# Performance work log

Measured on AMD Instinct MI355X. Metric: run time of the kernel, lower is better.

The kernel has to match this reference:

```python
import jax, jax.numpy as jnp
import numpy as np

SCALE_FACTOR = 4.0
DROPOUT_P = 0.5
DROPOUT_KEY = jax.random.key(42)  # fixed key: torch dropout is stochastic; we fix RNG for reproducibility


def setup_inputs() -> dict:
    key = jax.random.key(0)
    k1, k2 = jax.random.split(key)
    x1 = jax.random.normal(k1, (4096, 1024), dtype=jnp.float32)
    x2 = jax.random.normal(k2, (4096, 1024), dtype=jnp.float32)
    return {"x1": x1, "x2": x2}


def reference(x1, x2):
    # scores: [M, N] = x1 @ x2^T, scaled
    scores = jnp.matmul(x1, x2.T) * SCALE_FACTOR
    # F.softmax with no dim on 2-D input -> softmax over dim 1 (keys)
    attn = jax.nn.softmax(scores, axis=-1)
    # dropout p=0.5, train mode (inverted dropout: scale kept units by 1/(1-p))
    keep = jax.random.bernoulli(DROPOUT_KEY, 1.0 - DROPOUT_P, attn.shape)
    attn = jnp.where(keep, attn / (1.0 - DROPOUT_P), 0.0).astype(attn.dtype)
    # output: [M, D] = attn @ x2 (x2 reused as values)
    return jnp.matmul(attn, x2)
```

## Files before the change

### kernel.cpp

```cpp
#include <hip/hip_runtime.h>

typedef unsigned short u16;
typedef unsigned int   u32;
typedef __attribute__((ext_vector_type(4))) float f32x4;
typedef __attribute__((ext_vector_type(8))) short bf16x8;
typedef __attribute__((ext_vector_type(8))) unsigned short u16x8;
typedef __attribute__((ext_vector_type(4))) unsigned short u16x4;

#define MROWS 4096
#define DDIM  1024

__device__ __forceinline__ u16 f2bf(float f) {
  u32 u = __float_as_uint(f);
  return (u16)((u + 0x7FFFu + ((u >> 16) & 1u)) >> 16);
}
__device__ __forceinline__ float bf2f(u16 h) { return __uint_as_float(((u32)h) << 16); }

__device__ __forceinline__ u32 rotl32(u32 x, int r) { return (x << r) | (x >> (32 - r)); }
__device__ __forceinline__ u32 threefry_bits(u32 n) {
  const u32 K0 = 0u, K1 = 42u, K2 = 0x1BD11BDAu ^ 0u ^ 42u;
  u32 x0 = K0;
  u32 x1 = n + K1;
#define TF4(a,b,c,d) \
  x0 += x1; x1 = rotl32(x1, a); x1 ^= x0; \
  x0 += x1; x1 = rotl32(x1, b); x1 ^= x0; \
  x0 += x1; x1 = rotl32(x1, c); x1 ^= x0; \
  x0 += x1; x1 = rotl32(x1, d); x1 ^= x0;
  TF4(13,15,26,6);  x0 += K1; x1 += K2 + 1u;
  TF4(17,29,16,24); x0 += K2; x1 += K0 + 2u;
  TF4(13,15,26,6);  x0 += K0; x1 += K1 + 3u;
  TF4(17,29,16,24); x0 += K1; x1 += K2 + 4u;
  TF4(13,15,26,6);  x0 += K2; x1 += K0 + 5u;
#undef TF4
  return x0 ^ x1;
}

__global__ __launch_bounds__(256)
void expand3(const float4* __restrict__ x, u16* __restrict__ out, float scale, int patA,
             u32* __restrict__ mask, u32 wordBase) {
  int t = blockIdx.x * 256 + threadIdx.x;
  float4 v0 = x[(size_t)t * 2], v1 = x[(size_t)t * 2 + 1];
  float vv[8] = {v0.x*scale, v0.y*scale, v0.z*scale, v0.w*scale,
                 v1.x*scale, v1.y*scale, v1.z*scale, v1.w*scale};
  u16 o[24];
#pragma unroll
  for (int j = 0; j < 8; ++j) {
    u16 h = f2bf(vv[j]);
    u16 l = f2bf(vv[j] - bf2f(h));
    if (patA) { o[3*j]=h; o[3*j+1]=h; o[3*j+2]=l; }
    else      { o[3*j]=h; o[3*j+1]=l; o[3*j+2]=h; }
  }
  u16x8* dst = (u16x8*)(out + (size_t)t * 24);
#pragma unroll
  for (int q = 0; q < 3; ++q) {
    u16x8 wv;
#pragma unroll
    for (int j = 0; j < 8; ++j) wv[j] = o[q*8+j];
    dst[q] = wv;
  }
  u32 w = wordBase + ((u32)t >> 1);
  u32 sh = ((u32)t & 1u) << 4;
  u32 n0 = w * 32u + sh;
  u32 half = 0;
#pragma unroll 4
  for (int b = 0; b < 16; ++b) half |= (threefry_bits(n0 + (u32)b) >> 31) << (sh + b);
  u32 word = half | (u32)__shfl_xor((int)half, 1, 64);
  if ((t & 1) == 0) mask[w] = word;
}

__global__ __launch_bounds__(256)
void transpose_bf16(const float* __restrict__ x2, u16* __restrict__ VT) {
  __shared__ float tile[64][65];
  int tid = threadIdx.x;
  int dt = blockIdx.x;
  int kt = blockIdx.y;
#pragma unroll
  for (int it = 0; it < 16; ++it) {
    int lin = it * 256 + tid;
    int r = lin >> 6, c = lin & 63;
    tile[r][c] = x2[(size_t)(kt*64 + r) * DDIM + dt*64 + c];
  }
  __syncthreads();
#pragma unroll
  for (int it = 0; it < 16; ++it) {
    int lin = it * 256 + tid;
    int dr = lin >> 6, kc = lin & 63;
    VT[(size_t)(dt*64 + dr) * MROWS + kt*64 + kc] = f2bf(tile[kc][dr]);
  }
}

__device__ __forceinline__ void gload16(const u16* g, u16* l) {
  __builtin_amdgcn_global_load_lds(
      (const __attribute__((address_space(1))) void*)g,
      (__attribute__((address_space(3))) void*)l, 16, 0, 0);
}

#define BARRIER() do { asm volatile("" ::: "memory"); __builtin_amdgcn_s_barrier(); \
                       asm volatile("" ::: "memory"); } while (0)
#define VMCNT(N)  asm volatile("s_waitcnt vmcnt(" #N ")" ::: "memory")
#define PRIO1()   __builtin_amdgcn_s_setprio(1)
#define PRIO0()   __builtin_amdgcn_s_setprio(0)

__device__ __forceinline__ void mma_quad(f32x4 (&acc)[8][4], const bf16x8 (&aF)[4][2],
                                         const bf16x8 (&bF)[2][2], int MH, int NH) {
#pragma unroll
  for (int kx = 0; kx < 2; ++kx)
#pragma unroll
    for (int m = 0; m < 4; ++m)
#pragma unroll
      for (int n = 0; n < 2; ++n)
        acc[MH*4+m][NH*2+n] = __builtin_amdgcn_mfma_f32_16x16x32_bf16(
            aF[m][kx], bF[n][kx], acc[MH*4+m][NH*2+n], 0, 0, 0);
}

template <bool OUT16>
__global__ __launch_bounds__(512, 2)
void gemm256(const u16* __restrict__ A, const u16* __restrict__ Bt, void* __restrict__ Cv,
             int M, int N, int K, int ntpc) {
  __shared__ u16 smem[65536];
  const int tid = threadIdx.x;
  const int lane = tid & 63;
  const int w = tid >> 6;
  const int wr = w >> 2;
  const int wc = w & 3;
  const int fr = lane & 15;
  const int hi = lane >> 4;

  const long bm = (long)blockIdx.y * 256;
  const long bn = (long)blockIdx.x * 256;
  const size_t kcol0 = (size_t)blockIdx.z * ntpc * 64;

  const int srow = tid >> 3;
  const int scol = (((tid & 7) ^ (srow & 7)) << 3);
  const u16* Abase = A  + (size_t)(bm + srow) * K + kcol0 + scol;
  const u16* Bbase = Bt + (size_t)(bn + srow) * K + kcol0 + scol;

  const int csw0 = ((hi)     ^ (fr & 7)) << 3;
  const int csw1 = ((4 + hi) ^ (fr & 7)) << 3;
  const int arow = (wr*16 + fr) * 64;
  const int brow = (wc*16 + fr) * 64;

#define RD_A(dst, D, H) do { \
    const u16* _b0 = smem + ((D)*2+(H))*8192 + arow + csw0; \
    const u16* _b1 = smem + ((D)*2+(H))*8192 + arow + csw1; \
    dst[0][0] = *(const bf16x8*)(_b0);        dst[0][1] = *(const bf16x8*)(_b1); \
    dst[1][0] = *(const bf16x8*)(_b0 + 2048); dst[1][1] = *(const bf16x8*)(_b1 + 2048); \
    dst[2][0] = *(const bf16x8*)(_b0 + 4096); dst[2][1] = *(const bf16x8*)(_b1 + 4096); \
    dst[3][0] = *(const bf16x8*)(_b0 + 6144); dst[3][1] = *(const bf16x8*)(_b1 + 6144); } while (0)
#define RD_B(dst, D, H) do { \
    const u16* _b0 = smem + 32768 + ((D)*2+(H))*8192 + brow + csw0; \
    const u16* _b1 = smem + 32768 + ((D)*2+(H))*8192 + brow + csw1; \
    dst[0][0] = *(const bf16x8*)(_b0);        dst[0][1] = *(const bf16x8*)(_b1); \
    dst[1][0] = *(const bf16x8*)(_b0 + 4096); dst[1][1] = *(const bf16x8*)(_b1 + 4096); } while (0)

  f32x4 acc[8][4];
#pragma unroll
  for (int m = 0; m < 8; ++m)
#pragma unroll
    for (int n = 0; n < 4; ++n) acc[m][n] = (f32x4){0.f, 0.f, 0.f, 0.f};
  bf16x8 a0[4][2], a1[4][2], b0[2][2], b1[2][2];

#define STAGE_A(TAU,H,D) do { \
    const u16* _s = Abase + (size_t)(H)*128*K + (size_t)(TAU)*64; \
    u16* _d = smem + ((D)*2+(H))*8192 + tid*8; \
    gload16(_s, _d); gload16(_s + (size_t)64*K, _d + 4096); } while (0)
#define STAGE_B(TAU,H,D) do { \
    const u16* _s = Bbase + (size_t)(H)*128*K + (size_t)(TAU)*64; \
    u16* _d = smem + 32768 + ((D)*2+(H))*8192 + tid*8; \
    gload16(_s, _d); gload16(_s + (size_t)64*K, _d + 4096); } while (0)

  STAGE_A(0,0,0); STAGE_B(0,0,0);
  VMCNT(0); BARRIER();
  RD_A(a0, 0, 0); RD_B(b0, 0, 0);
  STAGE_B(0,1,0);
  STAGE_A(0,1,0);
  STAGE_A(1,0,1); STAGE_B(1,0,1);
  STAGE_B(1,1,1);
  STAGE_A(1,1,1);
  VMCNT(10); BARRIER();

  const int nt = ntpc;
  for (int T = 0; T < nt; T += 2) {
    const int t2 = (T + 2 < nt) ? T + 2 : nt - 1;
    const int t3 = (T + 3 < nt) ? T + 3 : nt - 1;

    RD_B(b1, 0, 1);
    PRIO1(); mma_quad(acc, a0, b0, 0, 0); PRIO0();
    VMCNT(8);  BARRIER();
    RD_A(a1, 0, 1);
    STAGE_A(t2, 0, 0); STAGE_B(t2, 0, 0);
    PRIO1(); mma_quad(acc, a0, b1, 0, 1); PRIO0();
    BARRIER();
    STAGE_B(t2, 1, 0);
    PRIO1(); mma_quad(acc, a1, b0, 1, 0); PRIO0();
    VMCNT(10); BARRIER();
    RD_A(a0, 1, 0); RD_B(b0, 1, 0);
    STAGE_A(t2, 1, 0);
    PRIO1(); mma_quad(acc, a1, b1, 1, 1); PRIO0();
    VMCNT(10); BARRIER();
    RD_B(b1, 1, 1);
    PRIO1(); mma_quad(acc, a0, b0, 0, 0); PRIO0();
    VMCNT(8);  BARRIER();
    RD_A(a1, 1, 1);
    STAGE_A(t3, 0, 1); STAGE_B(t3, 0, 1);
    PRIO1(); mma_quad(acc, a0, b1, 0, 1); PRIO0();
    BARRIER();
    STAGE_B(t3, 1, 1);
    PRIO1(); mma_quad(acc, a1, b0, 1, 0); PRIO0();
    VMCNT(10); BARRIER();
    RD_A(a0, 0, 0); RD_B(b0, 0, 0);
    STAGE_A(t3, 1, 1);
    PRIO1(); mma_quad(acc, a1, b1, 1, 1); PRIO0();
    VMCNT(10); BARRIER();
  }
#undef STAGE_A
#undef STAGE_B
#undef RD_A
#undef RD_B

#pragma unroll
  for (int m = 0; m < 8; ++m)
#pragma unroll
    for (int n = 0; n < 4; ++n) {
      size_t row0 = (size_t)(bm + m*32 + wr*16 + hi*4);
      size_t col  = (size_t)(bn + n*64 + wc*16 + fr);
#pragma unroll
      for (int r = 0; r < 4; ++r) {
        if (OUT16) {
          u16* Cz = (u16*)Cv + (size_t)blockIdx.z * (size_t)M * N;
          Cz[(row0 + r) * N + col] = f2bf(acc[m][n][r]);
        } else {
          float* Cz = (float*)Cv + (size_t)blockIdx.z * (size_t)M * N;
          Cz[(row0 + r) * N + col] = acc[m][n][r];
        }
      }
    }
}

__global__ __launch_bounds__(256)
void softmax_dropout(const float* __restrict__ S, const u32* __restrict__ mask,
                     u16* __restrict__ P) {
  const int tid  = threadIdx.x;
  const int lane = tid & 63;
  const int w    = tid >> 6;
  const int row  = blockIdx.x * 4 + w;
  const float4* Sr = (const float4*)(S + (size_t)row * MROWS);
  float4 v[16];
#pragma unroll
  for (int i = 0; i < 16; ++i) v[i] = Sr[i * 64 + lane];
  float m = -3.0e38f;
#pragma unroll
  for (int i = 0; i < 16; ++i)
    m = fmaxf(m, fmaxf(fmaxf(v[i].x, v[i].y), fmaxf(v[i].z, v[i].w)));
#pragma unroll
  for (int off = 32; off > 0; off >>= 1) m = fmaxf(m, __shfl_xor(m, off, 64));
  float s = 0.0f;
#pragma unroll
  for (int i = 0; i < 16; ++i) {
    v[i].x = __expf(v[i].x - m); v[i].y = __expf(v[i].y - m);
    v[i].z = __expf(v[i].z - m); v[i].w = __expf(v[i].w - m);
    s += v[i].x + v[i].y + v[i].z + v[i].w;
  }
#pragma unroll
  for (int off = 32; off > 0; off >>= 1) s += __shfl_xor(s, off, 64);
  const float inv = 2.0f / s;
  u16* Pr = P + (size_t)row * MROWS;
  const u32* Mw = mask + (size_t)row * 128;
#pragma unroll
  for (int i = 0; i < 16; ++i) {
    int j0 = (i * 64 + lane) * 4;
    u32 word = Mw[j0 >> 5];
    int sh = j0 & 31;
    float e[4] = {v[i].x, v[i].y, v[i].z, v[i].w};
    u16x4 o;
#pragma unroll
    for (int c = 0; c < 4; ++c) {
      float val = ((word >> (sh + c)) & 1u) ? 0.0f : e[c] * inv;
      o[c] = f2bf(val);
    }
    *(u16x4*)(Pr + j0) = o;
  }
}

__global__ __launch_bounds__(256)
void reduce4(const u16* __restrict__ p, float4* __restrict__ out) {
  size_t i = (size_t)blockIdx.x * 256 + threadIdx.x;
  const size_t NP = (size_t)MROWS * DDIM;
  u16x4 a = *(const u16x4*)(p + i*4);
  u16x4 b = *(const u16x4*)(p + NP + i*4);
  u16x4 c = *(const u16x4*)(p + 2*NP + i*4);
  u16x4 d = *(const u16x4*)(p + 3*NP + i*4);
  float4 r;
  r.x = bf2f(a[0]) + bf2f(b[0]) + bf2f(c[0]) + bf2f(d[0]);
  r.y = bf2f(a[1]) + bf2f(b[1]) + bf2f(c[1]) + bf2f(d[1]);
  r.z = bf2f(a[2]) + bf2f(b[2]) + bf2f(c[2]) + bf2f(d[2]);
  r.w = bf2f(a[3]) + bf2f(b[3]) + bf2f(c[3]) + bf2f(d[3]);
  out[i] = r;
}

extern "C" void kernel_launch(void* const* d_in, const int* in_sizes, int n_in,
                              void* d_out, int out_size, void* d_ws, size_t ws_size,
                              hipStream_t stream) {
  const float* x1 = (const float*)d_in[0];
  const float* x2 = (const float*)d_in[1];
  float* out = (float*)d_out;
  char* ws = (char*)d_ws;

  const size_t OFF_XB   = 25165824;
  const size_t OFF_VT   = 50331648;
  const size_t OFF_S    = 58720256;
  const size_t OFF_MASK = 125829120;
  const size_t NEED     = 127926272;
  if (ws_size < NEED) {
    hipMemsetAsync(d_out, 0x7F, (size_t)out_size * sizeof(float), stream);
    return;
  }
  u16*   XA = (u16*)(ws);
  u16*   XB = (u16*)(ws + OFF_XB);
  u16*   VT = (u16*)(ws + OFF_VT);
  float* S  = (float*)(ws + OFF_S);
  u16*   PT = (u16*)(ws + OFF_S);
  u32*   MK = (u32*)(ws + OFF_MASK);
  u16*   P  = (u16*)(ws);

  expand3<<<2048, 256, 0, stream>>>((const float4*)x1, XA, 4.0f, 1, MK, 0u);
  expand3<<<2048, 256, 0, stream>>>((const float4*)x2, XB, 1.0f, 0, MK, 262144u);
  transpose_bf16<<<dim3(16, 64), 256, 0, stream>>>(x2, VT);
  gemm256<false><<<dim3(16, 16, 1), 512, 0, stream>>>(XA, XB, S, 4096, 4096, 3072, 48);
  softmax_dropout<<<1024, 256, 0, stream>>>(S, MK, P);
  gemm256<true><<<dim3(4, 16, 4), 512, 0, stream>>>(P, VT, PT, 4096, 1024, 4096, 16);
  reduce4<<<4096, 256, 0, stream>>>(PT, (float4*)out);
}
```

Measured before the change: 192.0 us.

## Generate dropout mask inline in softmax, fuse x2 cast with transpose, remap PV grid

```diff
diff --git a/kernel.cpp b/kernel.cpp
--- a/kernel.cpp
+++ b/kernel.cpp
@@ -36,19 +36,17 @@
 }
 
 __global__ __launch_bounds__(256)
-void expand3(const float4* __restrict__ x, u16* __restrict__ out, float scale, int patA,
-             u32* __restrict__ mask, u32 wordBase) {
+void expandA(const float4* __restrict__ x, u16* __restrict__ out) {
   int t = blockIdx.x * 256 + threadIdx.x;
   float4 v0 = x[(size_t)t * 2], v1 = x[(size_t)t * 2 + 1];
-  float vv[8] = {v0.x*scale, v0.y*scale, v0.z*scale, v0.w*scale,
-                 v1.x*scale, v1.y*scale, v1.z*scale, v1.w*scale};
+  float vv[8] = {v0.x*4.f, v0.y*4.f, v0.z*4.f, v0.w*4.f,
+                 v1.x*4.f, v1.y*4.f, v1.z*4.f, v1.w*4.f};
   u16 o[24];
 #pragma unroll
   for (int j = 0; j < 8; ++j) {
     u16 h = f2bf(vv[j]);
     u16 l = f2bf(vv[j] - bf2f(h));
-    if (patA) { o[3*j]=h; o[3*j+1]=h; o[3*j+2]=l; }
-    else      { o[3*j]=h; o[3*j+1]=l; o[3*j+2]=h; }
+    o[3*j] = h; o[3*j+1] = h; o[3*j+2] = l;
   }
   u16x8* dst = (u16x8*)(out + (size_t)t * 24);
 #pragma unroll
@@ -58,18 +56,11 @@
     for (int j = 0; j < 8; ++j) wv[j] = o[q*8+j];
     dst[q] = wv;
   }
-  u32 w = wordBase + ((u32)t >> 1);
-  u32 sh = ((u32)t & 1u) << 4;
-  u32 n0 = w * 32u + sh;
-  u32 half = 0;
-#pragma unroll 4
-  for (int b = 0; b < 16; ++b) half |= (threefry_bits(n0 + (u32)b) >> 31) << (sh + b);
-  u32 word = half | (u32)__shfl_xor((int)half, 1, 64);
-  if ((t & 1) == 0) mask[w] = word;
 }
 
 __global__ __launch_bounds__(256)
-void transpose_bf16(const float* __restrict__ x2, u16* __restrict__ VT) {
+void castB_transpose(const float* __restrict__ x2, u16* __restrict__ XB,
+                     u16* __restrict__ VT) {
   __shared__ float tile[64][65];
   int tid = threadIdx.x;
   int dt = blockIdx.x;
@@ -81,6 +72,27 @@
     tile[r][c] = x2[(size_t)(kt*64 + r) * DDIM + dt*64 + c];
   }
   __syncthreads();
+#pragma unroll
+  for (int itr = 0; itr < 2; ++itr) {
+    int r  = (tid >> 3) + itr * 32;
+    int c0 = (tid & 7) * 8;
+    u16 o[24];
+#pragma unroll
+    for (int j = 0; j < 8; ++j) {
+      float v = tile[r][c0 + j];
+      u16 h = f2bf(v);
+      u16 l = f2bf(v - bf2f(h));
+      o[3*j] = h; o[3*j+1] = l; o[3*j+2] = h;
+    }
+    u16x8* dst = (u16x8*)(XB + (size_t)(kt*64 + r) * 3072 + (size_t)(dt*64 + c0) * 3);
+#pragma unroll
+    for (int q = 0; q < 3; ++q) {
+      u16x8 wv;
+#pragma unroll
+      for (int j = 0; j < 8; ++j) wv[j] = o[q*8+j];
+      dst[q] = wv;
+    }
+  }
 #pragma unroll
   for (int it = 0; it < 16; ++it) {
     int lin = it * 256 + tid;
@@ -113,7 +125,7 @@
             aF[m][kx], bF[n][kx], acc[MH*4+m][NH*2+n], 0, 0, 0);
 }
 
-template <bool OUT16>
+template <bool OUT16, bool REMAP>
 __global__ __launch_bounds__(512, 2)
 void gemm256(const u16* __restrict__ A, const u16* __restrict__ Bt, void* __restrict__ Cv,
              int M, int N, int K, int ntpc) {
@@ -126,8 +138,18 @@
   const int fr = lane & 15;
   const int hi = lane >> 4;
 
-  const long bm = (long)blockIdx.y * 256;
-  const long bn = (long)blockIdx.x * 256;
+  int bxi, byi;
+  if (REMAP) {
+    const int id0 = blockIdx.y * gridDim.x + blockIdx.x;
+    const int c = id0 & 7, j = id0 >> 3;
+    bxi = j >> 1;
+    byi = c * 2 + (j & 1);
+  } else {
+    bxi = blockIdx.x; byi = blockIdx.y;
+  }
+
+  const long bm = (long)byi * 256;
+  const long bn = (long)bxi * 256;
   const size_t kcol0 = (size_t)blockIdx.z * ntpc * 64;
 
   const int srow = tid >> 3;
@@ -238,8 +260,7 @@
 }
 
 __global__ __launch_bounds__(256)
-void softmax_dropout(const float* __restrict__ S, const u32* __restrict__ mask,
-                     u16* __restrict__ P) {
+void softmax_dropout(const float* __restrict__ S, u16* __restrict__ P) {
   const int tid  = threadIdx.x;
   const int lane = tid & 63;
   const int w    = tid >> 6;
@@ -265,17 +286,16 @@
   for (int off = 32; off > 0; off >>= 1) s += __shfl_xor(s, off, 64);
   const float inv = 2.0f / s;
   u16* Pr = P + (size_t)row * MROWS;
-  const u32* Mw = mask + (size_t)row * 128;
 #pragma unroll
   for (int i = 0; i < 16; ++i) {
     int j0 = (i * 64 + lane) * 4;
-    u32 word = Mw[j0 >> 5];
-    int sh = j0 & 31;
+    u32 base = (u32)row * 4096u + (u32)j0;
     float e[4] = {v[i].x, v[i].y, v[i].z, v[i].w};
     u16x4 o;
 #pragma unroll
     for (int c = 0; c < 4; ++c) {
-      float val = ((word >> (sh + c)) & 1u) ? 0.0f : e[c] * inv;
+      u32 bits = threefry_bits(base + (u32)c);
+      float val = (bits & 0x80000000u) ? 0.0f : e[c] * inv;
       o[c] = f2bf(val);
     }
     *(u16x4*)(Pr + j0) = o;
@@ -309,8 +329,7 @@
   const size_t OFF_XB   = 25165824;
   const size_t OFF_VT   = 50331648;
   const size_t OFF_S    = 58720256;
-  const size_t OFF_MASK = 125829120;
-  const size_t NEED     = 127926272;
+  const size_t NEED     = 125829120;
   if (ws_size < NEED) {
     hipMemsetAsync(d_out, 0x7F, (size_t)out_size * sizeof(float), stream);
     return;
@@ -320,14 +339,12 @@
   u16*   VT = (u16*)(ws + OFF_VT);
   float* S  = (float*)(ws + OFF_S);
   u16*   PT = (u16*)(ws + OFF_S);
-  u32*   MK = (u32*)(ws + OFF_MASK);
   u16*   P  = (u16*)(ws);
 
-  expand3<<<2048, 256, 0, stream>>>((const float4*)x1, XA, 4.0f, 1, MK, 0u);
-  expand3<<<2048, 256, 0, stream>>>((const float4*)x2, XB, 1.0f, 0, MK, 262144u);
-  transpose_bf16<<<dim3(16, 64), 256, 0, stream>>>(x2, VT);
-  gemm256<false><<<dim3(16, 16, 1), 512, 0, stream>>>(XA, XB, S, 4096, 4096, 3072, 48);
-  softmax_dropout<<<1024, 256, 0, stream>>>(S, MK, P);
-  gemm256<true><<<dim3(4, 16, 4), 512, 0, stream>>>(P, VT, PT, 4096, 1024, 4096, 16);
+  expandA<<<2048, 256, 0, stream>>>((const float4*)x1, XA);
+  castB_transpose<<<dim3(16, 64), 256, 0, stream>>>(x2, XB, VT);
+  gemm256<false, false><<<dim3(16, 16, 1), 512, 0, stream>>>(XA, XB, S, 4096, 4096, 3072, 48);
+  softmax_dropout<<<1024, 256, 0, stream>>>(S, P);
+  gemm256<true, true><<<dim3(4, 16, 4), 512, 0, stream>>>(P, VT, PT, 4096, 1024, 4096, 16);
   reduce4<<<4096, 256, 0, stream>>>(PT, (float4*)out);
 }
```

Result: faster. 187.0 us (-2.6%).
